# Performance work log

Measured on AMD Instinct MI355X. Metric: run time of the kernel, lower is better.

Reference implementation:

```python
import jax, jax.numpy as jnp
import numpy as np

D_MODEL = 768
N_EXPERTS = 16
FFN_HIDDEN = 3072
TOP_K = 4


def setup_inputs() -> dict:
    key = jax.random.key(0)
    k0, k1, k2, k3, k4 = jax.random.split(key, 5)
    scale = 0.02
    hidden_states = jax.random.normal(k0, (2, 512, D_MODEL), dtype=jnp.float32)
    router_w = jax.random.normal(k1, (N_EXPERTS, D_MODEL), dtype=jnp.float32) * scale
    w1 = jax.random.normal(k2, (N_EXPERTS, FFN_HIDDEN, D_MODEL), dtype=jnp.float32) * scale  # gate proj
    v1 = jax.random.normal(k3, (N_EXPERTS, FFN_HIDDEN, D_MODEL), dtype=jnp.float32) * scale  # up proj
    w2 = jax.random.normal(k4, (N_EXPERTS, D_MODEL, FFN_HIDDEN), dtype=jnp.float32) * scale  # down proj
    return {"hidden_states": hidden_states, "router_w": router_w, "w1": w1, "v1": v1, "w2": w2}


def reference(hidden_states, router_w, w1, v1, w2):
    orig_shape = hidden_states.shape
    x = hidden_states.reshape(-1, orig_shape[-1])  # [T, D]
    n_experts = router_w.shape[0]

    # Router: ReplicatedLinear, no bias -> logits [T, E]
    logits = x @ router_w.T
    # FusedMoE gating: softmax in fp32 over all experts, top-k, renormalize
    probs = jax.nn.softmax(logits.astype(jnp.float32), axis=-1)
    topk_w, topk_idx = jax.lax.top_k(probs, TOP_K)
    topk_w = topk_w / jnp.sum(topk_w, axis=-1, keepdims=True)
    # Dense per-(token, expert) combine weights [T, E]; zero for unselected experts
    dense_w = jnp.sum(
        jax.nn.one_hot(topk_idx, n_experts, dtype=x.dtype) * topk_w[..., None].astype(x.dtype),
        axis=1,
    )

    # Grouped expert SiLU-GLU FFN, expressed densely over experts (weights mask unselected)
    gate = jnp.einsum('td,eid->tei', x, w1)  # [T, E, I]
    up = jnp.einsum('td,eid->tei', x, v1)    # [T, E, I]
    act = jax.nn.silu(gate) * up
    out = jnp.einsum('tei,edi,te->td', act, w2, dense_w)  # weighted combine
    return out.reshape(orig_shape)
```

## Files before the change

kernel.cpp:

```cpp
#include <hip/hip_runtime.h>
#include <hip/hip_bf16.h>

#define NTOK 1024
#define DM 768
#define NEXP 16
#define FFN 3072
#define NSLOT 4096
#define SLOTPAD 4112

typedef __bf16 bf16x8 __attribute__((ext_vector_type(8)));
typedef float f32x4 __attribute__((ext_vector_type(4)));

static __device__ __forceinline__ unsigned short f2bf(float f){
  unsigned u = __builtin_bit_cast(unsigned, f);
  u += 0x7fffu + ((u >> 16) & 1u);
  return (unsigned short)(u >> 16);
}

__global__ void k_init(int* counts){
  if (threadIdx.x < NEXP) counts[threadIdx.x] = 0;
}

__global__ __launch_bounds__(64) void k_router(const float* __restrict__ x,
    const float* __restrict__ rw, int* counts, int* topk_e, float* topk_w){
  const int t = blockIdx.x;
  const int lane = threadIdx.x;
  float acc[NEXP];
  #pragma unroll
  for (int e = 0; e < NEXP; e++) acc[e] = 0.f;
  const float* xr = x + (size_t)t * DM;
  for (int d = lane; d < DM; d += 64){
    float xv = xr[d];
    #pragma unroll
    for (int e = 0; e < NEXP; e++) acc[e] = fmaf(xv, rw[e * DM + d], acc[e]);
  }
  #pragma unroll
  for (int e = 0; e < NEXP; e++){
    float v = acc[e];
    #pragma unroll
    for (int off = 32; off; off >>= 1) v += __shfl_xor(v, off, 64);
    acc[e] = v;
  }
  if (lane == 0){
    float mx = -1e30f;
    #pragma unroll
    for (int e = 0; e < NEXP; e++) mx = fmaxf(mx, acc[e]);
    float p[NEXP];
    #pragma unroll
    for (int e = 0; e < NEXP; e++) p[e] = __expf(acc[e] - mx);
    int ids[4]; float wv[4]; float wsum = 0.f;
    for (int k = 0; k < 4; k++){
      float best = -1.f; int bi = 0;
      #pragma unroll
      for (int e = 0; e < NEXP; e++) if (p[e] > best){ best = p[e]; bi = e; }
      ids[k] = bi; wv[k] = best; wsum += best; p[bi] = -2.f;
    }
    float inv = 1.f / wsum;
    for (int k = 0; k < 4; k++){
      topk_e[t * 4 + k] = ids[k];
      topk_w[t * 4 + k] = wv[k] * inv;
      atomicAdd(&counts[ids[k]], 1);
    }
  }
}

__global__ void k_offsets(const int* counts, int* offs, int* cursor){
  if (threadIdx.x == 0){
    int s = 0;
    for (int e = 0; e < NEXP; e++){ offs[e] = s; cursor[e] = s; s += counts[e]; }
    offs[NEXP] = s;
  }
}

__global__ __launch_bounds__(256) void k_assign(const int* __restrict__ topk_e,
    int* cursor, int* tokmap, int* tokslot){
  int t = blockIdx.x * 256 + threadIdx.x;
  if (t < NTOK){
    for (int k = 0; k < 4; k++){
      int e = topk_e[t * 4 + k];
      int pos = atomicAdd(&cursor[e], 1);
      tokmap[pos] = t;
      tokslot[t * 4 + k] = pos;
    }
  }
}

__global__ __launch_bounds__(192) void k_gather(const float* __restrict__ x,
    const int* __restrict__ tokmap, unsigned short* __restrict__ xg){
  const int s = blockIdx.x;
  const int j = threadIdx.x;
  const int t = tokmap[s];
  float4 v = reinterpret_cast<const float4*>(x + (size_t)t * DM)[j];
  ushort4 o; o.x = f2bf(v.x); o.y = f2bf(v.y); o.z = f2bf(v.z); o.w = f2bf(v.w);
  reinterpret_cast<ushort4*>(xg + (size_t)s * DM)[j] = o;
}

#define P1S 776
__global__ __launch_bounds__(256, 3) void k_ffn1(const float* __restrict__ w1,
    const float* __restrict__ v1, const unsigned short* __restrict__ xg,
    unsigned short* __restrict__ act, const int* __restrict__ offs){
  __shared__ unsigned short bw[2][16][P1S];
  const int e  = blockIdx.y;
  const int i0 = blockIdx.x * 16;
  const int tid = threadIdx.x;
  {
    const float* s0 = w1 + ((size_t)e * FFN + i0) * DM;
    const float* s1 = v1 + ((size_t)e * FFN + i0) * DM;
    #pragma unroll
    for (int tt = 0; tt < 12; tt++){
      int idx = tid + tt * 256;
      int row = idx / 192;
      int c4  = idx - row * 192;
      float4 a = *reinterpret_cast<const float4*>(s0 + (size_t)row * DM + c4 * 4);
      float4 b = *reinterpret_cast<const float4*>(s1 + (size_t)row * DM + c4 * 4);
      ushort4 oa; oa.x = f2bf(a.x); oa.y = f2bf(a.y); oa.z = f2bf(a.z); oa.w = f2bf(a.w);
      ushort4 ob; ob.x = f2bf(b.x); ob.y = f2bf(b.y); ob.z = f2bf(b.z); ob.w = f2bf(b.w);
      *reinterpret_cast<ushort4*>(&bw[0][row][c4 * 4]) = oa;
      *reinterpret_cast<ushort4*>(&bw[1][row][c4 * 4]) = ob;
    }
  }
  __syncthreads();
  const int base = offs[e];
  const int cnt  = offs[e + 1] - base;
  const int nmt  = (cnt + 15) >> 4;
  const int wid = tid >> 6, lane = tid & 63;
  const int n = lane & 15, quad = lane >> 4;
  const unsigned short* b0p = &bw[0][n][quad * 8];
  const unsigned short* b1p = &bw[1][n][quad * 8];
  for (int mt = wid; mt < nmt; mt += 4){
    const unsigned short* ap = xg + (size_t)(base + mt * 16 + n) * DM + quad * 8;
    f32x4 accg = {0.f, 0.f, 0.f, 0.f}, accu = {0.f, 0.f, 0.f, 0.f};
    #pragma unroll 4
    for (int k = 0; k < 24; k++){
      bf16x8 a = *reinterpret_cast<const bf16x8*>(ap + k * 32);
      bf16x8 g = *reinterpret_cast<const bf16x8*>(b0p + k * 32);
      bf16x8 u = *reinterpret_cast<const bf16x8*>(b1p + k * 32);
      accg = __builtin_amdgcn_mfma_f32_16x16x32_bf16(a, g, accg, 0, 0, 0);
      accu = __builtin_amdgcn_mfma_f32_16x16x32_bf16(a, u, accu, 0, 0, 0);
    }
    #pragma unroll
    for (int r = 0; r < 4; r++){
      int rowi = mt * 16 + quad * 4 + r;
      if (rowi < cnt){
        float gv = accg[r], uv = accu[r];
        float sv = gv / (1.f + __expf(-gv));
        act[(size_t)(base + rowi) * FFN + i0 + n] = f2bf(sv * uv);
      }
    }
  }
}

#define P2S 136
__global__ __launch_bounds__(256, 2) void k_ffn2(const float* __restrict__ w2,
    const unsigned short* __restrict__ act, float* __restrict__ outs,
    const int* __restrict__ offs){
  __shared__ unsigned short bs[2][32][P2S];
  const int e  = blockIdx.y;
  const int d0 = blockIdx.x * 32;
  const int tid = threadIdx.x;
  const int wid = tid >> 6, lane = tid & 63;
  const int n = lane & 15, quad = lane >> 4;
  const int base = offs[e];
  const int cnt  = offs[e + 1] - base;
  const int nsb  = (cnt + 319) / 320;
  const float* bsrc = w2 + ((size_t)e * DM + d0) * FFN;
  for (int sb = 0; sb < nsb; sb++){
    f32x4 acc[5][2];
    #pragma unroll
    for (int j = 0; j < 5; j++){
      acc[j][0] = (f32x4){0.f, 0.f, 0.f, 0.f};
      acc[j][1] = (f32x4){0.f, 0.f, 0.f, 0.f};
    }
    const unsigned short* actp[5];
    bool rok[5];
    #pragma unroll
    for (int j = 0; j < 5; j++){
      int rowbase = sb * 320 + (wid + j * 4) * 16;
      rok[j] = rowbase < cnt;
      actp[j] = act + (size_t)(base + rowbase + n) * FFN;
    }
    #pragma unroll
    for (int tt = 0; tt < 4; tt++){
      int idx = tid + tt * 256;
      int row = idx >> 5, kf = idx & 31;
      float4 v = *reinterpret_cast<const float4*>(bsrc + (size_t)row * FFN + kf * 4);
      ushort4 o; o.x = f2bf(v.x); o.y = f2bf(v.y); o.z = f2bf(v.z); o.w = f2bf(v.w);
      *reinterpret_cast<ushort4*>(&bs[0][row][kf * 4]) = o;
    }
    for (int kc = 0; kc < 24; kc++){
      const int cur = kc & 1;
      float4 pf[4];
      if (kc < 23){
        #pragma unroll
        for (int tt = 0; tt < 4; tt++){
          int idx = tid + tt * 256;
          int row = idx >> 5, kf = idx & 31;
          pf[tt] = *reinterpret_cast<const float4*>(bsrc + (size_t)row * FFN + (kc + 1) * 128 + kf * 4);
        }
      }
      __syncthreads();
      #pragma unroll
      for (int kl = 0; kl < 4; kl++){
        bf16x8 b0 = *reinterpret_cast<const bf16x8*>(&bs[cur][n][kl * 32 + quad * 8]);
        bf16x8 b1 = *reinterpret_cast<const bf16x8*>(&bs[cur][16 + n][kl * 32 + quad * 8]);
        #pragma unroll
        for (int j = 0; j < 5; j++){
          if (rok[j]){
            bf16x8 a = *reinterpret_cast<const bf16x8*>(actp[j] + kc * 128 + kl * 32 + quad * 8);
            acc[j][0] = __builtin_amdgcn_mfma_f32_16x16x32_bf16(a, b0, acc[j][0], 0, 0, 0);
            acc[j][1] = __builtin_amdgcn_mfma_f32_16x16x32_bf16(a, b1, acc[j][1], 0, 0, 0);
          }
        }
      }
      if (kc < 23){
        #pragma unroll
        for (int tt = 0; tt < 4; tt++){
          int idx = tid + tt * 256;
          int row = idx >> 5, kf = idx & 31;
          ushort4 o; o.x = f2bf(pf[tt].x); o.y = f2bf(pf[tt].y); o.z = f2bf(pf[tt].z); o.w = f2bf(pf[tt].w);
          *reinterpret_cast<ushort4*>(&bs[cur ^ 1][row][kf * 4]) = o;
        }
      }
    }
    #pragma unroll
    for (int j = 0; j < 5; j++){
      if (!rok[j]) continue;
      int rowbase = sb * 320 + (wid + j * 4) * 16;
      #pragma unroll
      for (int ct = 0; ct < 2; ct++){
        #pragma unroll
        for (int r = 0; r < 4; r++){
          int rowi = rowbase + quad * 4 + r;
          if (rowi < cnt)
            outs[(size_t)(base + rowi) * DM + d0 + ct * 16 + n] = acc[j][ct][r];
        }
      }
    }
  }
}

__global__ __launch_bounds__(192) void k_combine(const float* __restrict__ outs,
    const int* __restrict__ tokslot, const float* __restrict__ topk_w,
    float* __restrict__ out){
  const int t = blockIdx.x;
  const int j = threadIdx.x;
  float4 o = {0.f, 0.f, 0.f, 0.f};
  #pragma unroll
  for (int k = 0; k < 4; k++){
    int s = tokslot[t * 4 + k];
    float w = topk_w[t * 4 + k];
    float4 v = reinterpret_cast<const float4*>(outs + (size_t)s * DM)[j];
    o.x += w * v.x; o.y += w * v.y; o.z += w * v.z; o.w += w * v.w;
  }
  reinterpret_cast<float4*>(out + (size_t)t * DM)[j] = o;
}

#define WS_COUNTS  0
#define WS_OFFS    64
#define WS_CURSOR  192
#define WS_TOPKE   256
#define WS_TOPKW   (WS_TOPKE + NSLOT * 4)
#define WS_TOKSLOT (WS_TOPKW + NSLOT * 4)
#define WS_TOKMAP  (WS_TOKSLOT + NSLOT * 4)
#define WS_XG      131072
#define WS_ACT     (WS_XG + (size_t)SLOTPAD * DM * 2)
#define WS_OUTS    (WS_ACT + (size_t)SLOTPAD * FFN * 2)

extern "C" void kernel_launch(void* const* d_in, const int* in_sizes, int n_in,
                              void* d_out, int out_size, void* d_ws, size_t ws_size,
                              hipStream_t stream){
  const float* x  = (const float*)d_in[0];
  const float* rw = (const float*)d_in[1];
  const float* w1 = (const float*)d_in[2];
  const float* v1 = (const float*)d_in[3];
  const float* w2 = (const float*)d_in[4];
  float* out = (float*)d_out;
  char* ws = (char*)d_ws;

  int*   counts  = (int*)(ws + WS_COUNTS);
  int*   offs    = (int*)(ws + WS_OFFS);
  int*   cursor  = (int*)(ws + WS_CURSOR);
  int*   topk_e  = (int*)(ws + WS_TOPKE);
  float* topk_w  = (float*)(ws + WS_TOPKW);
  int*   tokslot = (int*)(ws + WS_TOKSLOT);
  int*   tokmap  = (int*)(ws + WS_TOKMAP);
  unsigned short* xg  = (unsigned short*)(ws + WS_XG);
  unsigned short* act = (unsigned short*)(ws + WS_ACT);
  float* outs = (float*)(ws + WS_OUTS);

  k_init<<<dim3(1), dim3(64), 0, stream>>>(counts);
  k_router<<<dim3(NTOK), dim3(64), 0, stream>>>(x, rw, counts, topk_e, topk_w);
  k_offsets<<<dim3(1), dim3(64), 0, stream>>>(counts, offs, cursor);
  k_assign<<<dim3(4), dim3(256), 0, stream>>>(topk_e, cursor, tokmap, tokslot);
  k_gather<<<dim3(NSLOT), dim3(192), 0, stream>>>(x, tokmap, xg);
  k_ffn1<<<dim3(FFN / 16, NEXP), dim3(256), 0, stream>>>(w1, v1, xg, act, offs);
  k_ffn2<<<dim3(DM / 32, NEXP), dim3(256), 0, stream>>>(w2, act, outs, offs);
  k_combine<<<dim3(NTOK), dim3(192), 0, stream>>>(outs, tokslot, topk_w, out);
}
```

Baseline: 739.0 us.

## Retile FFN1 with double-buffered K-chunks and fuse routing prep kernels

FFN1 now uses 32-column tiles. Weights are staged in 128-wide K chunks, double-buffered through LDS with register prefetch, and each wave computes up to five 16-row token tiles per 320-row superblock, so weight loads are reused across more tokens. Separately, the routing stage drops the init, offsets and assign kernels: counts are built in a single-block shared-memory histogram, and slot assignment is fused with the bf16 gather, one block per token. The router dot product is vectorised with float4 loads. This cuts launches and raises MFMA work per LDS load, at the cost of more registers and lower occupancy (launch bound goes from 3 to 2).

New measurement: 665.1 us. 1.11x faster.

```diff
diff --git a/kernel.cpp b/kernel.cpp
--- a/kernel.cpp
+++ b/kernel.cpp
@@ -17,22 +17,26 @@
   return (unsigned short)(u >> 16);
 }
 
-__global__ void k_init(int* counts){
-  if (threadIdx.x < NEXP) counts[threadIdx.x] = 0;
-}
-
 __global__ __launch_bounds__(64) void k_router(const float* __restrict__ x,
-    const float* __restrict__ rw, int* counts, int* topk_e, float* topk_w){
+    const float* __restrict__ rw, int* topk_e, float* topk_w){
   const int t = blockIdx.x;
   const int lane = threadIdx.x;
+  float4 xv[3];
+  const float4* xr = reinterpret_cast<const float4*>(x + (size_t)t * DM);
+  #pragma unroll
+  for (int i = 0; i < 3; i++) xv[i] = xr[lane + i * 64];
   float acc[NEXP];
   #pragma unroll
-  for (int e = 0; e < NEXP; e++) acc[e] = 0.f;
-  const float* xr = x + (size_t)t * DM;
-  for (int d = lane; d < DM; d += 64){
-    float xv = xr[d];
-    #pragma unroll
-    for (int e = 0; e < NEXP; e++) acc[e] = fmaf(xv, rw[e * DM + d], acc[e]);
+  for (int e = 0; e < NEXP; e++){
+    const float4* rp = reinterpret_cast<const float4*>(rw + e * DM);
+    float s = 0.f;
+    #pragma unroll
+    for (int i = 0; i < 3; i++){
+      float4 w = rp[lane + i * 64];
+      s = fmaf(xv[i].x, w.x, s); s = fmaf(xv[i].y, w.y, s);
+      s = fmaf(xv[i].z, w.z, s); s = fmaf(xv[i].w, w.w, s);
+    }
+    acc[e] = s;
   }
   #pragma unroll
   for (int e = 0; e < NEXP; e++){
@@ -59,92 +63,144 @@
     for (int k = 0; k < 4; k++){
       topk_e[t * 4 + k] = ids[k];
       topk_w[t * 4 + k] = wv[k] * inv;
-      atomicAdd(&counts[ids[k]], 1);
-    }
-  }
-}
-
-__global__ void k_offsets(const int* counts, int* offs, int* cursor){
-  if (threadIdx.x == 0){
+    }
+  }
+}
+
+__global__ __launch_bounds__(256) void k_prep(const int* __restrict__ topk_e,
+    int* offs, int* cursor){
+  __shared__ int cs[NEXP];
+  const int tid = threadIdx.x;
+  if (tid < NEXP) cs[tid] = 0;
+  __syncthreads();
+  for (int i = tid; i < NSLOT; i += 256) atomicAdd(&cs[topk_e[i]], 1);
+  __syncthreads();
+  if (tid == 0){
     int s = 0;
-    for (int e = 0; e < NEXP; e++){ offs[e] = s; cursor[e] = s; s += counts[e]; }
+    for (int e = 0; e < NEXP; e++){ offs[e] = s; cursor[e] = s; s += cs[e]; }
     offs[NEXP] = s;
   }
 }
 
-__global__ __launch_bounds__(256) void k_assign(const int* __restrict__ topk_e,
-    int* cursor, int* tokmap, int* tokslot){
-  int t = blockIdx.x * 256 + threadIdx.x;
-  if (t < NTOK){
-    for (int k = 0; k < 4; k++){
-      int e = topk_e[t * 4 + k];
-      int pos = atomicAdd(&cursor[e], 1);
-      tokmap[pos] = t;
-      tokslot[t * 4 + k] = pos;
-    }
-  }
-}
-
-__global__ __launch_bounds__(192) void k_gather(const float* __restrict__ x,
-    const int* __restrict__ tokmap, unsigned short* __restrict__ xg){
-  const int s = blockIdx.x;
-  const int j = threadIdx.x;
-  const int t = tokmap[s];
-  float4 v = reinterpret_cast<const float4*>(x + (size_t)t * DM)[j];
+__global__ __launch_bounds__(192) void k_assign_gather(const float* __restrict__ x,
+    const int* __restrict__ topk_e, int* cursor, int* tokslot,
+    unsigned short* __restrict__ xg){
+  __shared__ int slot_s[4];
+  const int t = blockIdx.x;
+  const int tid = threadIdx.x;
+  if (tid < 4){
+    int e = topk_e[t * 4 + tid];
+    int pos = atomicAdd(&cursor[e], 1);
+    slot_s[tid] = pos;
+    tokslot[t * 4 + tid] = pos;
+  }
+  __syncthreads();
+  float4 v = reinterpret_cast<const float4*>(x + (size_t)t * DM)[tid];
   ushort4 o; o.x = f2bf(v.x); o.y = f2bf(v.y); o.z = f2bf(v.z); o.w = f2bf(v.w);
-  reinterpret_cast<ushort4*>(xg + (size_t)s * DM)[j] = o;
-}
-
-#define P1S 776
-__global__ __launch_bounds__(256, 3) void k_ffn1(const float* __restrict__ w1,
+  #pragma unroll
+  for (int k = 0; k < 4; k++)
+    reinterpret_cast<ushort4*>(xg + (size_t)slot_s[k] * DM)[tid] = o;
+}
+
+#define P1K 136
+__global__ __launch_bounds__(256, 2) void k_ffn1(const float* __restrict__ w1,
     const float* __restrict__ v1, const unsigned short* __restrict__ xg,
     unsigned short* __restrict__ act, const int* __restrict__ offs){
-  __shared__ unsigned short bw[2][16][P1S];
+  __shared__ unsigned short bs[2][2][32][P1K];
   const int e  = blockIdx.y;
-  const int i0 = blockIdx.x * 16;
+  const int i0 = blockIdx.x * 32;
   const int tid = threadIdx.x;
-  {
-    const float* s0 = w1 + ((size_t)e * FFN + i0) * DM;
-    const float* s1 = v1 + ((size_t)e * FFN + i0) * DM;
-    #pragma unroll
-    for (int tt = 0; tt < 12; tt++){
-      int idx = tid + tt * 256;
-      int row = idx / 192;
-      int c4  = idx - row * 192;
-      float4 a = *reinterpret_cast<const float4*>(s0 + (size_t)row * DM + c4 * 4);
-      float4 b = *reinterpret_cast<const float4*>(s1 + (size_t)row * DM + c4 * 4);
-      ushort4 oa; oa.x = f2bf(a.x); oa.y = f2bf(a.y); oa.z = f2bf(a.z); oa.w = f2bf(a.w);
-      ushort4 ob; ob.x = f2bf(b.x); ob.y = f2bf(b.y); ob.z = f2bf(b.z); ob.w = f2bf(b.w);
-      *reinterpret_cast<ushort4*>(&bw[0][row][c4 * 4]) = oa;
-      *reinterpret_cast<ushort4*>(&bw[1][row][c4 * 4]) = ob;
-    }
-  }
-  __syncthreads();
+  const int wid = tid >> 6, lane = tid & 63;
+  const int n = lane & 15, quad = lane >> 4;
   const int base = offs[e];
   const int cnt  = offs[e + 1] - base;
-  const int nmt  = (cnt + 15) >> 4;
-  const int wid = tid >> 6, lane = tid & 63;
-  const int n = lane & 15, quad = lane >> 4;
-  const unsigned short* b0p = &bw[0][n][quad * 8];
-  const unsigned short* b1p = &bw[1][n][quad * 8];
-  for (int mt = wid; mt < nmt; mt += 4){
-    const unsigned short* ap = xg + (size_t)(base + mt * 16 + n) * DM + quad * 8;
-    f32x4 accg = {0.f, 0.f, 0.f, 0.f}, accu = {0.f, 0.f, 0.f, 0.f};
-    #pragma unroll 4
-    for (int k = 0; k < 24; k++){
-      bf16x8 a = *reinterpret_cast<const bf16x8*>(ap + k * 32);
-      bf16x8 g = *reinterpret_cast<const bf16x8*>(b0p + k * 32);
-      bf16x8 u = *reinterpret_cast<const bf16x8*>(b1p + k * 32);
-      accg = __builtin_amdgcn_mfma_f32_16x16x32_bf16(a, g, accg, 0, 0, 0);
-      accu = __builtin_amdgcn_mfma_f32_16x16x32_bf16(a, u, accu, 0, 0, 0);
-    }
-    #pragma unroll
-    for (int r = 0; r < 4; r++){
-      int rowi = mt * 16 + quad * 4 + r;
-      if (rowi < cnt){
-        float gv = accg[r], uv = accu[r];
-        float sv = gv / (1.f + __expf(-gv));
-        act[(size_t)(base + rowi) * FFN + i0 + n] = f2bf(sv * uv);
+  const int nsb  = (cnt + 319) / 320;
+  const float* srcs[2] = { w1 + ((size_t)e * FFN + i0) * DM,
+                           v1 + ((size_t)e * FFN + i0) * DM };
+  int srow[4], skf[4];
+  #pragma unroll
+  for (int tt = 0; tt < 4; tt++){ int idx = tid + tt * 256; srow[tt] = idx >> 5; skf[tt] = idx & 31; }
+
+  for (int sb = 0; sb < nsb; sb++){
+    f32x4 accg[5][2], accu[5][2];
+    #pragma unroll
+    for (int j = 0; j < 5; j++){
+      accg[j][0] = (f32x4){0,0,0,0}; accg[j][1] = (f32x4){0,0,0,0};
+      accu[j][0] = (f32x4){0,0,0,0}; accu[j][1] = (f32x4){0,0,0,0};
+    }
+    const unsigned short* ap[5]; bool rok[5];
+    #pragma unroll
+    for (int j = 0; j < 5; j++){
+      int rb = sb * 320 + (wid + j * 4) * 16;
+      rok[j] = rb < cnt;
+      ap[j] = xg + (size_t)(base + rb + n) * DM;
+    }
+    #pragma unroll
+    for (int m = 0; m < 2; m++){
+      #pragma unroll
+      for (int tt = 0; tt < 4; tt++){
+        float4 v = reinterpret_cast<const float4*>(srcs[m] + (size_t)srow[tt] * DM)[skf[tt]];
+        ushort4 o; o.x = f2bf(v.x); o.y = f2bf(v.y); o.z = f2bf(v.z); o.w = f2bf(v.w);
+        *reinterpret_cast<ushort4*>(&bs[0][m][srow[tt]][skf[tt] * 4]) = o;
+      }
+    }
+    for (int kc = 0; kc < 6; kc++){
+      const int cur = kc & 1;
+      float4 pf[8];
+      if (kc < 5){
+        #pragma unroll
+        for (int m = 0; m < 2; m++)
+          #pragma unroll
+          for (int tt = 0; tt < 4; tt++)
+            pf[m * 4 + tt] = reinterpret_cast<const float4*>(
+                srcs[m] + (size_t)srow[tt] * DM)[(kc + 1) * 32 + skf[tt]];
+      }
+      __syncthreads();
+      #pragma unroll
+      for (int kl = 0; kl < 4; kl++){
+        const int ko = kl * 32 + quad * 8;
+        bf16x8 bg0 = *reinterpret_cast<const bf16x8*>(&bs[cur][0][n][ko]);
+        bf16x8 bg1 = *reinterpret_cast<const bf16x8*>(&bs[cur][0][16 + n][ko]);
+        bf16x8 bu0 = *reinterpret_cast<const bf16x8*>(&bs[cur][1][n][ko]);
+        bf16x8 bu1 = *reinterpret_cast<const bf16x8*>(&bs[cur][1][16 + n][ko]);
+        #pragma unroll
+        for (int j = 0; j < 5; j++){
+          if (rok[j]){
+            bf16x8 a = *reinterpret_cast<const bf16x8*>(ap[j] + kc * 128 + ko);
+            accg[j][0] = __builtin_amdgcn_mfma_f32_16x16x32_bf16(a, bg0, accg[j][0], 0, 0, 0);
+            accg[j][1] = __builtin_amdgcn_mfma_f32_16x16x32_bf16(a, bg1, accg[j][1], 0, 0, 0);
+            accu[j][0] = __builtin_amdgcn_mfma_f32_16x16x32_bf16(a, bu0, accu[j][0], 0, 0, 0);
+            accu[j][1] = __builtin_amdgcn_mfma_f32_16x16x32_bf16(a, bu1, accu[j][1], 0, 0, 0);
+          }
+        }
+      }
+      if (kc < 5){
+        #pragma unroll
+        for (int m = 0; m < 2; m++){
+          #pragma unroll
+          for (int tt = 0; tt < 4; tt++){
+            float4 v = pf[m * 4 + tt];
+            ushort4 o; o.x = f2bf(v.x); o.y = f2bf(v.y); o.z = f2bf(v.z); o.w = f2bf(v.w);
+            *reinterpret_cast<ushort4*>(&bs[cur ^ 1][m][srow[tt]][skf[tt] * 4]) = o;
+          }
+        }
+      }
+    }
+    #pragma unroll
+    for (int j = 0; j < 5; j++){
+      if (!rok[j]) continue;
+      int rb = sb * 320 + (wid + j * 4) * 16;
+      #pragma unroll
+      for (int ct = 0; ct < 2; ct++){
+        #pragma unroll
+        for (int r = 0; r < 4; r++){
+          int rowi = rb + quad * 4 + r;
+          if (rowi < cnt){
+            float gv = accg[j][ct][r], uv = accu[j][ct][r];
+            float sv = gv / (1.f + __expf(-gv));
+            act[(size_t)(base + rowi) * FFN + i0 + ct * 16 + n] = f2bf(sv * uv);
+          }
+        }
       }
     }
   }
@@ -255,13 +311,11 @@
   reinterpret_cast<float4*>(out + (size_t)t * DM)[j] = o;
 }
 
-#define WS_COUNTS  0
 #define WS_OFFS    64
 #define WS_CURSOR  192
 #define WS_TOPKE   256
 #define WS_TOPKW   (WS_TOPKE + NSLOT * 4)
 #define WS_TOKSLOT (WS_TOPKW + NSLOT * 4)
-#define WS_TOKMAP  (WS_TOKSLOT + NSLOT * 4)
 #define WS_XG      131072
 #define WS_ACT     (WS_XG + (size_t)SLOTPAD * DM * 2)
 #define WS_OUTS    (WS_ACT + (size_t)SLOTPAD * FFN * 2)
@@ -277,23 +331,19 @@
   float* out = (float*)d_out;
   char* ws = (char*)d_ws;
 
-  int*   counts  = (int*)(ws + WS_COUNTS);
   int*   offs    = (int*)(ws + WS_OFFS);
   int*   cursor  = (int*)(ws + WS_CURSOR);
   int*   topk_e  = (int*)(ws + WS_TOPKE);
   float* topk_w  = (float*)(ws + WS_TOPKW);
   int*   tokslot = (int*)(ws + WS_TOKSLOT);
-  int*   tokmap  = (int*)(ws + WS_TOKMAP);
   unsigned short* xg  = (unsigned short*)(ws + WS_XG);
   unsigned short* act = (unsigned short*)(ws + WS_ACT);
   float* outs = (float*)(ws + WS_OUTS);
 
-  k_init<<<dim3(1), dim3(64), 0, stream>>>(counts);
-  k_router<<<dim3(NTOK), dim3(64), 0, stream>>>(x, rw, counts, topk_e, topk_w);
-  k_offsets<<<dim3(1), dim3(64), 0, stream>>>(counts, offs, cursor);
-  k_assign<<<dim3(4), dim3(256), 0, stream>>>(topk_e, cursor, tokmap, tokslot);
-  k_gather<<<dim3(NSLOT), dim3(192), 0, stream>>>(x, tokmap, xg);
-  k_ffn1<<<dim3(FFN / 16, NEXP), dim3(256), 0, stream>>>(w1, v1, xg, act, offs);
+  k_router<<<dim3(NTOK), dim3(64), 0, stream>>>(x, rw, topk_e, topk_w);
+  k_prep<<<dim3(1), dim3(256), 0, stream>>>(topk_e, offs, cursor);
+  k_assign_gather<<<dim3(NTOK), dim3(192), 0, stream>>>(x, topk_e, cursor, tokslot, xg);
+  k_ffn1<<<dim3(FFN / 32, NEXP), dim3(256), 0, stream>>>(w1, v1, xg, act, offs);
   k_ffn2<<<dim3(DM / 32, NEXP), dim3(256), 0, stream>>>(w2, act, outs, offs);
   k_combine<<<dim3(NTOK), dim3(192), 0, stream>>>(outs, tokslot, topk_w, out);
 }
```
